# Performance work log

Measured on AMD Instinct MI355X. Metric: run time of the kernel, lower is better.

Reference implementation:

```python
import jax, jax.numpy as jnp
import numpy as np

B, S, D_MODEL, N_HEADS, HIDDEN = 4, 2048, 1024, 16, 4096
D_HEAD = D_MODEL // N_HEADS
LN_EPS = 1e-5


def setup_inputs() -> dict:
    key = jax.random.key(0)
    ks = jax.random.split(key, 20)
    s = 0.02
    return {
        "X": jax.random.normal(ks[0], (B, S, D_MODEL), dtype=jnp.float32),
        # attention projections (stored [in, out]; y = x @ W + b)
        "Wq": jax.random.normal(ks[1], (D_MODEL, D_MODEL), dtype=jnp.float32) * s,
        "bq": jnp.zeros((D_MODEL,), jnp.float32),
        "Wk": jax.random.normal(ks[2], (D_MODEL, D_MODEL), dtype=jnp.float32) * s,
        "bk": jnp.zeros((D_MODEL,), jnp.float32),
        "Wv": jax.random.normal(ks[3], (D_MODEL, D_MODEL), dtype=jnp.float32) * s,
        "bv": jnp.zeros((D_MODEL,), jnp.float32),
        "Wo": jax.random.normal(ks[4], (D_MODEL, D_MODEL), dtype=jnp.float32) * s,
        "bo": jnp.zeros((D_MODEL,), jnp.float32),
        # layernorm 1
        "g1": jnp.ones((D_MODEL,), jnp.float32),
        "beta1": jnp.zeros((D_MODEL,), jnp.float32),
        # FFN
        "W1": jax.random.normal(ks[5], (D_MODEL, HIDDEN), dtype=jnp.float32) * s,
        "b1": jnp.zeros((HIDDEN,), jnp.float32),
        "W2": jax.random.normal(ks[6], (HIDDEN, D_MODEL), dtype=jnp.float32) * s,
        "b2": jnp.zeros((D_MODEL,), jnp.float32),
        # layernorm 2
        "g2": jnp.ones((D_MODEL,), jnp.float32),
        "beta2": jnp.zeros((D_MODEL,), jnp.float32),
    }


def _layer_norm(x, gamma, beta):
    mu = jnp.mean(x, axis=-1, keepdims=True)
    var = jnp.mean(jnp.square(x - mu), axis=-1, keepdims=True)
    return (x - mu) * jax.lax.rsqrt(var + LN_EPS) * gamma + beta


def reference(X, Wq, bq, Wk, bk, Wv, bv, Wo, bo, g1, beta1, W1, b1, W2, b2, g2, beta2):
    b, s, d = X.shape
    # multi-head attention (dropout is identity in eval mode)
    q = (X @ Wq + bq).reshape(b, s, N_HEADS, D_HEAD)
    k = (X @ Wk + bk).reshape(b, s, N_HEADS, D_HEAD)
    v = (X @ Wv + bv).reshape(b, s, N_HEADS, D_HEAD)
    scale = 1.0 / np.sqrt(D_HEAD).astype(np.float32)
    scores = jnp.einsum('bqhd,bkhd->bhqk', q, k) * scale
    attn = jax.nn.softmax(scores, axis=-1)
    ctx = jnp.einsum('bhqk,bkhd->bqhd', attn, v).reshape(b, s, d)
    attn_out = ctx @ Wo + bo
    # AddNorm 1
    Y = _layer_norm(X + attn_out, g1, beta1)
    # FFN
    ffn_out = jax.nn.relu(Y @ W1 + b1) @ W2 + b2
    # AddNorm 2
    return _layer_norm(Y + ffn_out, g2, beta2)
```

## Files before the change

### kernel.cpp

```cpp
#include <hip/hip_runtime.h>
#include <stdint.h>

typedef unsigned short u16;
typedef short bf16x8 __attribute__((ext_vector_type(8)));
typedef float f32x4 __attribute__((ext_vector_type(4)));
typedef u16 u16x4 __attribute__((ext_vector_type(4)));
typedef u16 u16x8 __attribute__((ext_vector_type(8)));

#define LOG2E 1.4426950408889634f
#define QSCALE (0.125f * LOG2E)

__device__ __forceinline__ u16 f2bf(float f) {
  union { float f; uint32_t u; } x; x.f = f;
  uint32_t r = x.u + 0x7fffu + ((x.u >> 16) & 1u);
  return (u16)(r >> 16);
}
__device__ __forceinline__ u16 f2bf_ru(float f) {
  union { float f; uint32_t u; } x; x.f = f;
  return (u16)((x.u + 0x8000u) >> 16);
}
__device__ __forceinline__ float bf2f(u16 h) {
  union { uint32_t u; float f; } x; x.u = ((uint32_t)h) << 16;
  return x.f;
}
__device__ __forceinline__ uint32_t cvtpk(float lo, float hi) {
  uint32_t r;
  asm("v_cvt_pk_bf16_f32 %0, %1, %2" : "=v"(r) : "v"(lo), "v"(hi));
  return r;
}
__device__ __forceinline__ int swz3(int row) { return (row ^ (row >> 3)) & 7; }

__device__ __forceinline__ void gload_lds16(const void* g, void* lds) {
  __builtin_amdgcn_global_load_lds(
      (const __attribute__((address_space(1))) void*)g,
      (__attribute__((address_space(3))) void*)lds, 16, 0, 0);
}

__global__ __launch_bounds__(256) void cast_bf16(const float* __restrict__ in,
                                                 u16* __restrict__ out, int n8) {
  int i = blockIdx.x * 256 + threadIdx.x;
  const int stride = gridDim.x * 256;
  for (; i < n8; i += stride) {
    const f32x4* p = (const f32x4*)in + (size_t)i * 2;
    f32x4 a = p[0], b = p[1];
    u16x8 o;
    o[0] = f2bf(a[0]); o[1] = f2bf(a[1]); o[2] = f2bf(a[2]); o[3] = f2bf(a[3]);
    o[4] = f2bf(b[0]); o[5] = f2bf(b[1]); o[6] = f2bf(b[2]); o[7] = f2bf(b[3]);
    ((u16x8*)out)[i] = o;
  }
}

__global__ __launch_bounds__(256) void concat3(const float* __restrict__ a,
                                               const float* __restrict__ b,
                                               const float* __restrict__ c,
                                               float* __restrict__ o) {
  int i = blockIdx.x * 256 + threadIdx.x;
  if (i < 3072)
    o[i] = i < 1024 ? a[i] * QSCALE : (i < 2048 ? b[i - 1024] : c[i - 2048]);
}

__global__ __launch_bounds__(256) void transpose_cast(const float* __restrict__ in,
                                                      u16* __restrict__ out, int R, int C,
                                                      float scale) {
  __shared__ float tile[32][33];
  const int bc = blockIdx.x * 32, br = blockIdx.y * 32;
  const int tx = threadIdx.x & 31, ty = threadIdx.x >> 5;
#pragma unroll
  for (int i = 0; i < 32; i += 8)
    tile[ty + i][tx] = in[(size_t)(br + ty + i) * C + bc + tx];
  __syncthreads();
#pragma unroll
  for (int i = 0; i < 32; i += 8)
    out[(size_t)(bc + ty + i) * R + br + tx] = f2bf(tile[tx][ty + i] * scale);
}

__global__ __launch_bounds__(256) void vtrans(const u16* __restrict__ QKV,
                                              u16* __restrict__ Vtg) {
  __shared__ u16 tl[64][65];
  const int t = threadIdx.x;
  const int sblk = blockIdx.x, h = blockIdx.y, b = blockIdx.z;
  const int s0 = sblk * 64;
  const size_t ibase = ((size_t)b * 2048) * 3072 + 2048 + h * 64;
#pragma unroll
  for (int i = 0; i < 2; i++) {
    const int idx = i * 256 + t;
    const int sl = idx >> 3, d0 = (idx & 7) * 8;
    bf16x8 v = *(const bf16x8*)&QKV[ibase + (size_t)(s0 + sl) * 3072 + d0];
#pragma unroll
    for (int e = 0; e < 8; e++) tl[d0 + e][sl] = (u16)v[e];
  }
  __syncthreads();
  const size_t ob = ((size_t)(b * 16 + h) * 64) * 2048;
#pragma unroll
  for (int i = 0; i < 2; i++) {
    const int idx = i * 256 + t;
    const int r = idx >> 3, c0 = (idx & 7) * 8;
    u16x8 o;
#pragma unroll
    for (int e = 0; e < 8; e++) o[e] = tl[r][c0 + e];
    *(u16x8*)&Vtg[ob + (size_t)r * 2048 + s0 + c0] = o;
  }
}

template <int RELU>
__global__ __launch_bounds__(256) void gemm_bt(const u16* __restrict__ A,
                                               const u16* __restrict__ BT,
                                               const float* __restrict__ bias,
                                               u16* __restrict__ Cb,
                                               int M, int N, int K) {
  constexpr int BM = 128, BN = 128, BK = 64;
  __shared__ u16 As[BM * BK];
  __shared__ u16 Bs[BN * BK];
  const int t = threadIdx.x;
  const int w = t >> 6, lane = t & 63;
  const int la = lane & 15, lb = lane >> 4;
  const int wr = w >> 1, wc = w & 1;
  const int m0 = blockIdx.y * BM, n0 = blockIdx.x * BN;

  f32x4 acc[4][4];
#pragma unroll
  for (int i = 0; i < 4; i++)
#pragma unroll
    for (int j = 0; j < 4; j++) acc[i][j] = (f32x4){0.f, 0.f, 0.f, 0.f};

  for (int kt = 0; kt < K; kt += BK) {
#pragma unroll
    for (int i = 0; i < 4; i++) {
      const int s = i * 256 + t;
      const int row = s >> 3, col = (s & 7) * 8;
      gload_lds16(A + (size_t)(m0 + row) * K + kt + col, &As[(i * 256 + w * 64) * 8]);
      gload_lds16(BT + (size_t)(n0 + row) * K + kt + col, &Bs[(i * 256 + w * 64) * 8]);
    }
    __syncthreads();
#pragma unroll
    for (int ks = 0; ks < 2; ks++) {
      bf16x8 af[4], bfr[4];
#pragma unroll
      for (int i = 0; i < 4; i++)
        af[i] = *(const bf16x8*)&As[(wr * 64 + i * 16 + la) * BK + ks * 32 + lb * 8];
#pragma unroll
      for (int j = 0; j < 4; j++)
        bfr[j] = *(const bf16x8*)&Bs[(wc * 64 + j * 16 + la) * BK + ks * 32 + lb * 8];
#pragma unroll
      for (int i = 0; i < 4; i++)
#pragma unroll
        for (int j = 0; j < 4; j++)
          acc[i][j] = __builtin_amdgcn_mfma_f32_16x16x32_bf16(af[i], bfr[j], acc[i][j], 0, 0, 0);
    }
    __syncthreads();
  }
#pragma unroll
  for (int i = 0; i < 4; i++) {
    const int r = m0 + wr * 64 + i * 16 + lb * 4;
#pragma unroll
    for (int j = 0; j < 4; j++) {
      const int c = n0 + wc * 64 + j * 16 + la;
      const float bv = bias[c];
#pragma unroll
      for (int rr = 0; rr < 4; rr++) {
        float v = acc[i][j][rr] + bv;
        if (RELU) v = fmaxf(v, 0.f);
        Cb[(size_t)(r + rr) * N + c] = f2bf(v);
      }
    }
  }
}

template <int RELU>
__global__ __launch_bounds__(512, 2) void gemm8p(const u16* __restrict__ A,
                                                 const u16* __restrict__ BT,
                                                 const float* __restrict__ bias,
                                                 u16* __restrict__ Cb,
                                                 int M, int N, int K, int nbx) {
  __shared__ u16 As[2][256 * 64];
  __shared__ u16 Bs[2][256 * 64];
  const int t = threadIdx.x;
  const int w = t >> 6, lane = t & 63;
  const int la = lane & 15, lb = lane >> 4;
  const int wr = w >> 2, wc = w & 3;
  int bid = (int)blockIdx.x;
  const int cpx = (int)gridDim.x >> 3;
  bid = (bid & 7) * cpx + (bid >> 3);
  const int m0 = (bid / nbx) * 256, n0 = (bid % nbx) * 256;
  const int NT = K >> 6;
  const int row64 = t >> 3;
  const int colp = ((t & 7) ^ swz3(row64)) << 3;

#define STG_A(buf, tile, q) \
  gload_lds16(A + (size_t)(m0 + (q)*64 + row64) * K + ((tile) << 6) + colp, \
              &As[buf][(q)*4096 + w * 512])
#define STG_B(buf, tile, q) \
  gload_lds16(BT + (size_t)(n0 + (q)*64 + row64) * K + ((tile) << 6) + colp, \
              &Bs[buf][(q)*4096 + w * 512])
#define LDA(dst, mf, ks) { const int r_ = wr * 128 + (mf)*16 + la; \
  dst = *(const bf16x8*)&As[cur][r_ * 64 + (((((ks) << 2) + lb) ^ swz3(r_)) << 3)]; }
#define LDB(dst, nf, ks) { const int r_ = wc * 64 + (nf)*16 + la; \
  dst = *(const bf16x8*)&Bs[cur][r_ * 64 + (((((ks) << 2) + lb) ^ swz3(r_)) << 3)]; }
#define MFMA16(mh, nh, barr) \
  __builtin_amdgcn_s_setprio(1); \
  _Pragma("unroll") for (int ks = 0; ks < 2; ks++) \
  _Pragma("unroll") for (int i = 0; i < 4; i++) \
  _Pragma("unroll") for (int j = 0; j < 2; j++) \
    acc[(mh)*4 + i][(nh)*2 + j] = __builtin_amdgcn_mfma_f32_16x16x32_bf16( \
        af[i][ks], barr[j][ks], acc[(mh)*4 + i][(nh)*2 + j], 0, 0, 0); \
  __builtin_amdgcn_s_setprio(0);
#define BAR1() __builtin_amdgcn_s_barrier(); \
  asm volatile("s_waitcnt lgkmcnt(0)" ::: "memory"); \
  __builtin_amdgcn_sched_barrier(0)

  f32x4 acc[8][4];
#pragma unroll
  for (int i = 0; i < 8; i++)
#pragma unroll
    for (int j = 0; j < 4; j++) acc[i][j] = (f32x4){0.f, 0.f, 0.f, 0.f};

  STG_A(0, 0, 0); STG_A(0, 0, 2);
  STG_B(0, 0, 0); STG_B(0, 0, 1); STG_B(0, 0, 2); STG_B(0, 0, 3);
  STG_A(0, 0, 1); STG_A(0, 0, 3);
  asm volatile("s_waitcnt vmcnt(2)" ::: "memory");
  __builtin_amdgcn_s_barrier();

  for (int tile = 0; tile < NT; ++tile) {
    const int cur = tile & 1, nxt = cur ^ 1;
    const bool hn = (tile + 1) < NT;
    bf16x8 af[4][2], b0[2][2], b1[2][2];
#pragma unroll
    for (int i = 0; i < 4; i++) { LDA(af[i][0], i, 0); LDA(af[i][1], i, 1); }
#pragma unroll
    for (int j = 0; j < 2; j++) { LDB(b0[j][0], j, 0); LDB(b0[j][1], j, 1); }
    if (hn) { STG_A(nxt, tile + 1, 0); STG_A(nxt, tile + 1, 2); }
    BAR1();
    MFMA16(0, 0, b0);
    __builtin_amdgcn_s_barrier();
#pragma unroll
    for (int j = 0; j < 2; j++) { LDB(b1[j][0], 2 + j, 0); LDB(b1[j][1], 2 + j, 1); }
    if (hn) { STG_B(nxt, tile + 1, 0); STG_B(nxt, tile + 1, 1); }
    BAR1();
    MFMA16(0, 1, b1);
    if (hn) { asm volatile("s_waitcnt vmcnt(4)" ::: "memory"); }
    else    { asm volatile("s_waitcnt vmcnt(0)" ::: "memory"); }
    __builtin_amdgcn_s_barrier();
#pragma unroll
    for (int i = 0; i < 4; i++) { LDA(af[i][0], 4 + i, 0); LDA(af[i][1], 4 + i, 1); }
    if (hn) { STG_B(nxt, tile + 1, 2); STG_B(nxt, tile + 1, 3); }
    BAR1();
    MFMA16(1, 0, b0);
    __builtin_amdgcn_s_barrier();
    if (hn) { STG_A(nxt, tile + 1, 1); STG_A(nxt, tile + 1, 3); }
    BAR1();
    MFMA16(1, 1, b1);
    if (hn) { asm volatile("s_waitcnt vmcnt(2)" ::: "memory"); }
    __builtin_amdgcn_s_barrier();
  }
#undef STG_A
#undef STG_B
#undef LDA
#undef LDB
#undef MFMA16
#undef BAR1

#pragma unroll
  for (int mf = 0; mf < 8; mf++) {
    const int r = m0 + wr * 128 + mf * 16 + lb * 4;
#pragma unroll
    for (int nf = 0; nf < 4; nf++) {
      const int c = n0 + wc * 64 + nf * 16 + la;
      const float bv = bias[c];
#pragma unroll
      for (int rr = 0; rr < 4; rr++) {
        float v = acc[mf][nf][rr] + bv;
        if (RELU) v = fmaxf(v, 0.f);
        Cb[(size_t)(r + rr) * N + c] = f2bf(v);
      }
    }
  }
}

__global__ __launch_bounds__(256) void attn_fwd(const u16* __restrict__ Qg,
                                                const u16* __restrict__ Kg,
                                                const u16* __restrict__ Vtg,
                                                u16* __restrict__ Og, int LDM) {
  constexpr int S = 2048, DMO = 1024, NT = S / 64;
  __shared__ u16 Ks[2][64 * 64];
  __shared__ u16 Vt[2][64 * 64];
  const int t = threadIdx.x, w = t >> 6, lane = t & 63;
  const int la = lane & 15, lb = lane >> 4;
  const int qb = blockIdx.x, h = blockIdx.y, b = blockIdx.z;
  const size_t base = ((size_t)b * S) * LDM + h * 64;
  const size_t vbase = ((size_t)(b * 16 + h) * 64) * 2048;
  const size_t obase = ((size_t)b * S) * DMO + h * 64;
  const int qrow0 = qb * 128 + w * 32;
  const int sl0 = la + 32 * (lb & 1), sl1 = sl0 + 16;
  const int jsel = lb >> 1;

#define ATT_STAGE(buf, kt_) { \
  _Pragma("unroll") for (int i = 0; i < 2; i++) { \
    const int s = i * 256 + t; const int r = s >> 3; const int cg = s & 7; \
    gload_lds16(Kg + base + (size_t)((kt_) + r) * LDM + ((cg ^ swz3(r)) << 3), \
                &Ks[buf][s * 8]); } \
  _Pragma("unroll") for (int i = 0; i < 2; i++) { \
    const int s = i * 256 + t; const int r = s >> 3; const int cg = s & 7; \
    gload_lds16(Vtg + vbase + (size_t)r * 2048 + (kt_) + ((cg ^ swz3(r)) << 3), \
                &Vt[buf][s * 8]); } }

  bf16x8 qf[2][2];
#pragma unroll
  for (int rf = 0; rf < 2; rf++)
#pragma unroll
    for (int ks = 0; ks < 2; ks++)
      qf[rf][ks] = *(const bf16x8*)&Qg[base + (size_t)(qrow0 + rf * 16 + la) * LDM + ks * 32 + lb * 8];

  f32x4 accO[2][4];
  float m[2], l[2];
#pragma unroll
  for (int i = 0; i < 2; i++) {
    m[i] = -1e30f; l[i] = 0.f;
#pragma unroll
    for (int j = 0; j < 4; j++) accO[i][j] = (f32x4){0.f, 0.f, 0.f, 0.f};
  }

  ATT_STAGE(0, 0);
  asm volatile("s_waitcnt vmcnt(0)" ::: "memory");
  __builtin_amdgcn_s_barrier();

  for (int kt = 0; kt < NT; ++kt) {
    const int cur = kt & 1;
    if (kt + 1 < NT) ATT_STAGE(cur ^ 1, (kt + 1) * 64);

    f32x4 st[4][2];
#pragma unroll
    for (int j = 0; j < 4; j++)
#pragma unroll
      for (int rf = 0; rf < 2; rf++) st[j][rf] = (f32x4){0.f, 0.f, 0.f, 0.f};
    __builtin_amdgcn_s_setprio(1);
#pragma unroll
    for (int ks = 0; ks < 2; ks++) {
      bf16x8 kf[4];
#pragma unroll
      for (int j = 0; j < 4; j++) {
        const int r = j * 16 + la;
        kf[j] = *(const bf16x8*)&Ks[cur][r * 64 + ((((ks << 2) + lb) ^ swz3(r)) << 3)];
      }
#pragma unroll
      for (int j = 0; j < 4; j++)
#pragma unroll
        for (int rf = 0; rf < 2; rf++)
          st[j][rf] = __builtin_amdgcn_mfma_f32_16x16x32_bf16(kf[j], qf[rf][ks], st[j][rf], 0, 0, 0);
    }
    __builtin_amdgcn_s_setprio(0);

    bf16x8 pf[2][2];
#pragma unroll
    for (int rf = 0; rf < 2; rf++) {
      float rm = st[0][rf][0];
#pragma unroll
      for (int j = 0; j < 4; j++)
#pragma unroll
        for (int rr = 0; rr < 4; rr++) rm = fmaxf(rm, st[j][rf][rr]);
      if (__any(rm > m[rf] + 8.0f)) {
        rm = fmaxf(rm, __shfl_xor(rm, 16, 64));
        rm = fmaxf(rm, __shfl_xor(rm, 32, 64));
        const float mN = fmaxf(m[rf], rm);
        const float al = exp2f(m[rf] - mN);
        m[rf] = mN;
        l[rf] *= al;
#pragma unroll
        for (int rr = 0; rr < 4; rr++) {
          const float alr = __shfl(al, (lb << 2) + rr, 64);
#pragma unroll
          for (int cf = 0; cf < 4; cf++) accO[rf][cf][rr] *= alr;
        }
      }
      uint32_t wl[4], wh[4];
#pragma unroll
      for (int j = 0; j < 4; j++) {
        float p0 = exp2f(st[j][rf][0] - m[rf]);
        float p1 = exp2f(st[j][rf][1] - m[rf]);
        float p2 = exp2f(st[j][rf][2] - m[rf]);
        float p3 = exp2f(st[j][rf][3] - m[rf]);
        l[rf] += (p0 + p1) + (p2 + p3);
        wl[j] = cvtpk(p0, p1);
        wh[j] = cvtpk(p2, p3);
      }
#pragma unroll
      for (int ks = 0; ks < 2; ks++) {
        const int j0 = 2 * ks, j1 = 2 * ks + 1;
        uint32_t a0 = __shfl(wl[j0], sl0, 64), a1 = __shfl(wh[j0], sl0, 64);
        uint32_t a2 = __shfl(wl[j0], sl1, 64), a3 = __shfl(wh[j0], sl1, 64);
        uint32_t b0 = __shfl(wl[j1], sl0, 64), b1 = __shfl(wh[j1], sl0, 64);
        uint32_t b2 = __shfl(wl[j1], sl1, 64), b3 = __shfl(wh[j1], sl1, 64);
        union { uint32_t u[4]; bf16x8 v; } pk;
        pk.u[0] = jsel ? b0 : a0;
        pk.u[1] = jsel ? b1 : a1;
        pk.u[2] = jsel ? b2 : a2;
        pk.u[3] = jsel ? b3 : a3;
        pf[rf][ks] = pk.v;
      }
    }

    __builtin_amdgcn_s_setprio(1);
#pragma unroll
    for (int ks = 0; ks < 2; ks++) {
      bf16x8 vf[4];
#pragma unroll
      for (int cf = 0; cf < 4; cf++) {
        const int dr = cf * 16 + la;
        vf[cf] = *(const bf16x8*)&Vt[cur][dr * 64 + ((((ks << 2) + lb) ^ swz3(dr)) << 3)];
      }
#pragma unroll
      for (int rf = 0; rf < 2; rf++)
#pragma unroll
        for (int cf = 0; cf < 4; cf++)
          accO[rf][cf] = __builtin_amdgcn_mfma_f32_16x16x32_bf16(pf[rf][ks], vf[cf], accO[rf][cf], 0, 0, 0);
    }
    __builtin_amdgcn_s_setprio(0);

    asm volatile("s_waitcnt vmcnt(0)" ::: "memory");
    __builtin_amdgcn_s_barrier();
  }
#undef ATT_STAGE

#pragma unroll
  for (int rf = 0; rf < 2; rf++) {
    float l2 = l[rf];
    l2 += __shfl_xor(l2, 16, 64);
    l2 += __shfl_xor(l2, 32, 64);
    const float inv = 1.0f / l2;
#pragma unroll
    for (int rr = 0; rr < 4; rr++) {
      const float invr = __shfl(inv, (lb << 2) + rr, 64);
      const int r = qrow0 + rf * 16 + lb * 4 + rr;
#pragma unroll
      for (int cf = 0; cf < 4; cf++)
        Og[obase + (size_t)r * DMO + cf * 16 + la] = f2bf_ru(accO[rf][cf][rr] * invr);
    }
  }
}

template <int AF32, int OUTF32>
__global__ __launch_bounds__(256) void add_ln(const void* __restrict__ Ap,
                                              const u16* __restrict__ Bb,
                                              const float* __restrict__ g,
                                              const float* __restrict__ be,
                                              void* __restrict__ Yp) {
  constexpr int D = 1024;
  const int row = blockIdx.x, t = threadIdx.x;
  f32x4 a;
  if (AF32) {
    a = ((const f32x4*)((const float*)Ap + (size_t)row * D))[t];
  } else {
    u16x4 av = ((const u16x4*)((const u16*)Ap + (size_t)row * D))[t];
#pragma unroll
    for (int i = 0; i < 4; i++) a[i] = bf2f(av[i]);
  }
  u16x4 bv16 = ((const u16x4*)(Bb + (size_t)row * D))[t];
  f32x4 x;
#pragma unroll
  for (int i = 0; i < 4; i++) x[i] = a[i] + bf2f(bv16[i]);
  float s1 = x[0] + x[1] + x[2] + x[3];
  float s2 = x[0] * x[0] + x[1] * x[1] + x[2] * x[2] + x[3] * x[3];
#pragma unroll
  for (int off = 32; off > 0; off >>= 1) {
    s1 += __shfl_down(s1, off, 64);
    s2 += __shfl_down(s2, off, 64);
  }
  __shared__ float sm[8];
  const int w = t >> 6, lane = t & 63;
  if (lane == 0) { sm[w] = s1; sm[4 + w] = s2; }
  __syncthreads();
  s1 = sm[0] + sm[1] + sm[2] + sm[3];
  s2 = sm[4] + sm[5] + sm[6] + sm[7];
  const float mean = s1 * (1.0f / D);
  const float var = s2 * (1.0f / D) - mean * mean;
  const float rstd = rsqrtf(var + 1e-5f);
  const f32x4 gv = ((const f32x4*)g)[t];
  const f32x4 bv = ((const f32x4*)be)[t];
  f32x4 y;
#pragma unroll
  for (int i = 0; i < 4; i++) y[i] = (x[i] - mean) * rstd * gv[i] + bv[i];
  if (OUTF32) {
    ((f32x4*)((float*)Yp + (size_t)row * D))[t] = y;
  } else {
    u16x4 o;
#pragma unroll
    for (int i = 0; i < 4; i++) o[i] = f2bf(y[i]);
    ((u16x4*)((u16*)Yp + (size_t)row * D))[t] = o;
  }
}

extern "C" void kernel_launch(void* const* d_in, const int* in_sizes, int n_in,
                              void* d_out, int out_size, void* d_ws, size_t ws_size,
                              hipStream_t stream) {
  const float* X   = (const float*)d_in[0];
  const float* Wq  = (const float*)d_in[1];
  const float* bq  = (const float*)d_in[2];
  const float* Wk  = (const float*)d_in[3];
  const float* bk  = (const float*)d_in[4];
  const float* Wv  = (const float*)d_in[5];
  const float* bv  = (const float*)d_in[6];
  const float* Wo  = (const float*)d_in[7];
  const float* bo  = (const float*)d_in[8];
  const float* g1  = (const float*)d_in[9];
  const float* be1 = (const float*)d_in[10];
  const float* W1  = (const float*)d_in[11];
  const float* b1  = (const float*)d_in[12];
  const float* W2  = (const float*)d_in[13];
  const float* b2  = (const float*)d_in[14];
  const float* g2  = (const float*)d_in[15];
  const float* be2 = (const float*)d_in[16];

  const size_t MB = 1ull << 20;
  char* wsb = (char*)d_ws;
  u16*   WqkvT = (u16*)(wsb + 0 * MB);
  u16*   WoT   = (u16*)(wsb + 6 * MB);
  u16*   W1T   = (u16*)(wsb + 8 * MB);
  u16*   W2T   = (u16*)(wsb + 16 * MB);
  u16*   Xb    = (u16*)(wsb + 24 * MB);
  u16*   Ab    = (u16*)(wsb + 24 * MB);
  u16*   Fb    = (u16*)(wsb + 24 * MB);
  u16*   QKVb  = (u16*)(wsb + 40 * MB);
  u16*   Hb    = (u16*)(wsb + 40 * MB);
  float* bqkv  = (float*)(wsb + 88 * MB);
  u16*   Cx    = (u16*)(wsb + 88 * MB);
  u16*   Vt_g  = (u16*)(wsb + 104 * MB);
  u16*   Yb    = (u16*)(wsb + 104 * MB);
  (void)ws_size; (void)in_sizes; (void)n_in; (void)out_size;

  cast_bf16<<<2048, 256, 0, stream>>>(X, Xb, 8192 * 1024 / 8);
  concat3<<<12, 256, 0, stream>>>(bq, bk, bv, bqkv);
  transpose_cast<<<dim3(32, 32), 256, 0, stream>>>(Wq, WqkvT, 1024, 1024, QSCALE);
  transpose_cast<<<dim3(32, 32), 256, 0, stream>>>(Wk, WqkvT + 1024 * 1024, 1024, 1024, 1.0f);
  transpose_cast<<<dim3(32, 32), 256, 0, stream>>>(Wv, WqkvT + 2 * 1024 * 1024, 1024, 1024, 1.0f);
  transpose_cast<<<dim3(32, 32), 256, 0, stream>>>(Wo, WoT, 1024, 1024, 1.0f);
  transpose_cast<<<dim3(128, 32), 256, 0, stream>>>(W1, W1T, 1024, 4096, 1.0f);
  transpose_cast<<<dim3(32, 128), 256, 0, stream>>>(W2, W2T, 4096, 1024, 1.0f);

  gemm8p<0><<<384, 512, 0, stream>>>(Xb, WqkvT, bqkv, QKVb, 8192, 3072, 1024, 12);

  vtrans<<<dim3(32, 16, 4), 256, 0, stream>>>(QKVb, Vt_g);
  attn_fwd<<<dim3(16, 16, 4), 256, 0, stream>>>(QKVb, QKVb + 1024, Vt_g, Cx, 3072);

  gemm_bt<0><<<dim3(8, 64), 256, 0, stream>>>(Cx, WoT, bo, Ab, 8192, 1024, 1024);
  add_ln<1, 0><<<8192, 256, 0, stream>>>(X, Ab, g1, be1, Yb);
  gemm8p<1><<<512, 512, 0, stream>>>(Yb, W1T, b1, Hb, 8192, 4096, 1024, 16);
  gemm_bt<0><<<dim3(8, 64), 256, 0, stream>>>(Hb, W2T, b2, Fb, 8192, 1024, 4096);
  add_ln<0, 1><<<8192, 256, 0, stream>>>(Yb, Fb, g2, be2, d_out);
}
```

Baseline: 489.3 us.

## Switch attention to 32x32x16 MFMA with permlane P repack and MFMA row sums

Rewrites the attention inner loop to use 32x32x16 bf16 MFMAs, so each wave handles one 32-row query tile with a single running max instead of two 16-row tiles. The P matrix is repacked for the PV product with v_permlane32_swap instead of many cross-lane shuffles. The softmax denominator is accumulated by an extra MFMA against a ones vector instead of scalar adds. A launch-bounds occupancy hint of 3 is added. This aims to cut shuffle and VALU overhead in the softmax stage, at the cost of an extra MFMA per k-block and bf16-rounded row sums.

```diff
diff --git a/kernel.cpp b/kernel.cpp
--- a/kernel.cpp
+++ b/kernel.cpp
@@ -4,6 +4,7 @@
 typedef unsigned short u16;
 typedef short bf16x8 __attribute__((ext_vector_type(8)));
 typedef float f32x4 __attribute__((ext_vector_type(4)));
+typedef float f32x16 __attribute__((ext_vector_type(16)));
 typedef u16 u16x4 __attribute__((ext_vector_type(4)));
 typedef u16 u16x8 __attribute__((ext_vector_type(8)));
 
@@ -276,22 +277,20 @@
   }
 }
 
-__global__ __launch_bounds__(256) void attn_fwd(const u16* __restrict__ Qg,
-                                                const u16* __restrict__ Kg,
-                                                const u16* __restrict__ Vtg,
-                                                u16* __restrict__ Og, int LDM) {
+__global__ __launch_bounds__(256, 3) void attn_fwd(const u16* __restrict__ Qg,
+                                                   const u16* __restrict__ Kg,
+                                                   const u16* __restrict__ Vtg,
+                                                   u16* __restrict__ Og, int LDM) {
   constexpr int S = 2048, DMO = 1024, NT = S / 64;
   __shared__ u16 Ks[2][64 * 64];
   __shared__ u16 Vt[2][64 * 64];
   const int t = threadIdx.x, w = t >> 6, lane = t & 63;
-  const int la = lane & 15, lb = lane >> 4;
+  const int l5 = lane & 31, hf = lane >> 5;
   const int qb = blockIdx.x, h = blockIdx.y, b = blockIdx.z;
   const size_t base = ((size_t)b * S) * LDM + h * 64;
   const size_t vbase = ((size_t)(b * 16 + h) * 64) * 2048;
   const size_t obase = ((size_t)b * S) * DMO + h * 64;
   const int qrow0 = qb * 128 + w * 32;
-  const int sl0 = la + 32 * (lb & 1), sl1 = sl0 + 16;
-  const int jsel = lb >> 1;
 
 #define ATT_STAGE(buf, kt_) { \
   _Pragma("unroll") for (int i = 0; i < 2; i++) { \
@@ -303,21 +302,19 @@
     gload_lds16(Vtg + vbase + (size_t)r * 2048 + (kt_) + ((cg ^ swz3(r)) << 3), \
                 &Vt[buf][s * 8]); } }
 
-  bf16x8 qf[2][2];
-#pragma unroll
-  for (int rf = 0; rf < 2; rf++)
-#pragma unroll
-    for (int ks = 0; ks < 2; ks++)
-      qf[rf][ks] = *(const bf16x8*)&Qg[base + (size_t)(qrow0 + rf * 16 + la) * LDM + ks * 32 + lb * 8];
-
-  f32x4 accO[2][4];
-  float m[2], l[2];
-#pragma unroll
-  for (int i = 0; i < 2; i++) {
-    m[i] = -1e30f; l[i] = 0.f;
-#pragma unroll
-    for (int j = 0; j < 4; j++) accO[i][j] = (f32x4){0.f, 0.f, 0.f, 0.f};
-  }
+  bf16x8 qf[4];
+#pragma unroll
+  for (int kb = 0; kb < 4; kb++)
+    qf[kb] = *(const bf16x8*)&Qg[base + (size_t)(qrow0 + l5) * LDM + kb * 16 + hf * 8];
+
+  f32x16 accO0, accO1, accL;
+#pragma unroll
+  for (int i = 0; i < 16; i++) { accO0[i] = 0.f; accO1[i] = 0.f; accL[i] = 0.f; }
+  float m = -1e30f;
+
+  bf16x8 ones;
+#pragma unroll
+  for (int i = 0; i < 8; i++) ones[i] = (short)0x3F80;
 
   ATT_STAGE(0, 0);
   asm volatile("s_waitcnt vmcnt(0)" ::: "memory");
@@ -327,91 +324,75 @@
     const int cur = kt & 1;
     if (kt + 1 < NT) ATT_STAGE(cur ^ 1, (kt + 1) * 64);
 
-    f32x4 st[4][2];
-#pragma unroll
-    for (int j = 0; j < 4; j++)
-#pragma unroll
-      for (int rf = 0; rf < 2; rf++) st[j][rf] = (f32x4){0.f, 0.f, 0.f, 0.f};
+    f32x16 st0, st1;
+#pragma unroll
+    for (int i = 0; i < 16; i++) { st0[i] = 0.f; st1[i] = 0.f; }
     __builtin_amdgcn_s_setprio(1);
 #pragma unroll
-    for (int ks = 0; ks < 2; ks++) {
-      bf16x8 kf[4];
-#pragma unroll
-      for (int j = 0; j < 4; j++) {
-        const int r = j * 16 + la;
-        kf[j] = *(const bf16x8*)&Ks[cur][r * 64 + ((((ks << 2) + lb) ^ swz3(r)) << 3)];
+    for (int kb = 0; kb < 4; kb++) {
+      const int r0 = l5, r1 = 32 + l5;
+      bf16x8 kf0 = *(const bf16x8*)&Ks[cur][r0 * 64 + (((hf + 2 * kb) ^ swz3(r0)) << 3)];
+      bf16x8 kf1 = *(const bf16x8*)&Ks[cur][r1 * 64 + (((hf + 2 * kb) ^ swz3(r1)) << 3)];
+      st0 = __builtin_amdgcn_mfma_f32_32x32x16_bf16(kf0, qf[kb], st0, 0, 0, 0);
+      st1 = __builtin_amdgcn_mfma_f32_32x32x16_bf16(kf1, qf[kb], st1, 0, 0, 0);
+    }
+    __builtin_amdgcn_s_setprio(0);
+
+    float rm = st0[0];
+#pragma unroll
+    for (int i = 1; i < 16; i++) rm = fmaxf(rm, st0[i]);
+#pragma unroll
+    for (int i = 0; i < 16; i++) rm = fmaxf(rm, st1[i]);
+    if (__any(rm > m + 8.0f)) {
+      float ra = rm, rb = rm;
+      asm volatile("v_permlane32_swap_b32 %0, %1" : "+v"(ra), "+v"(rb));
+      rm = fmaxf(rm, fmaxf(ra, rb));
+      const float mN = fmaxf(m, rm);
+      const float al = exp2f(m - mN);
+      m = mN;
+#pragma unroll
+      for (int r = 0; r < 16; r++) {
+        const float alr = __shfl(al, (r & 3) + 8 * (r >> 2) + 4 * hf, 64);
+        accO0[r] *= alr; accO1[r] *= alr; accL[r] *= alr;
       }
-#pragma unroll
-      for (int j = 0; j < 4; j++)
-#pragma unroll
-        for (int rf = 0; rf < 2; rf++)
-          st[j][rf] = __builtin_amdgcn_mfma_f32_16x16x32_bf16(kf[j], qf[rf][ks], st[j][rf], 0, 0, 0);
-    }
-    __builtin_amdgcn_s_setprio(0);
-
-    bf16x8 pf[2][2];
-#pragma unroll
-    for (int rf = 0; rf < 2; rf++) {
-      float rm = st[0][rf][0];
-#pragma unroll
-      for (int j = 0; j < 4; j++)
-#pragma unroll
-        for (int rr = 0; rr < 4; rr++) rm = fmaxf(rm, st[j][rf][rr]);
-      if (__any(rm > m[rf] + 8.0f)) {
-        rm = fmaxf(rm, __shfl_xor(rm, 16, 64));
-        rm = fmaxf(rm, __shfl_xor(rm, 32, 64));
-        const float mN = fmaxf(m[rf], rm);
-        const float al = exp2f(m[rf] - mN);
-        m[rf] = mN;
-        l[rf] *= al;
-#pragma unroll
-        for (int rr = 0; rr < 4; rr++) {
-          const float alr = __shfl(al, (lb << 2) + rr, 64);
-#pragma unroll
-          for (int cf = 0; cf < 4; cf++) accO[rf][cf][rr] *= alr;
-        }
-      }
-      uint32_t wl[4], wh[4];
-#pragma unroll
-      for (int j = 0; j < 4; j++) {
-        float p0 = exp2f(st[j][rf][0] - m[rf]);
-        float p1 = exp2f(st[j][rf][1] - m[rf]);
-        float p2 = exp2f(st[j][rf][2] - m[rf]);
-        float p3 = exp2f(st[j][rf][3] - m[rf]);
-        l[rf] += (p0 + p1) + (p2 + p3);
-        wl[j] = cvtpk(p0, p1);
-        wh[j] = cvtpk(p2, p3);
-      }
-#pragma unroll
-      for (int ks = 0; ks < 2; ks++) {
-        const int j0 = 2 * ks, j1 = 2 * ks + 1;
-        uint32_t a0 = __shfl(wl[j0], sl0, 64), a1 = __shfl(wh[j0], sl0, 64);
-        uint32_t a2 = __shfl(wl[j0], sl1, 64), a3 = __shfl(wh[j0], sl1, 64);
-        uint32_t b0 = __shfl(wl[j1], sl0, 64), b1 = __shfl(wh[j1], sl0, 64);
-        uint32_t b2 = __shfl(wl[j1], sl1, 64), b3 = __shfl(wh[j1], sl1, 64);
-        union { uint32_t u[4]; bf16x8 v; } pk;
-        pk.u[0] = jsel ? b0 : a0;
-        pk.u[1] = jsel ? b1 : a1;
-        pk.u[2] = jsel ? b2 : a2;
-        pk.u[3] = jsel ? b3 : a3;
-        pf[rf][ks] = pk.v;
-      }
+    }
+
+    uint32_t pw0[8], pw1[8];
+#pragma unroll
+    for (int r2 = 0; r2 < 8; r2++) {
+      pw0[r2] = cvtpk(exp2f(st0[2 * r2] - m), exp2f(st0[2 * r2 + 1] - m));
+      pw1[r2] = cvtpk(exp2f(st1[2 * r2] - m), exp2f(st1[2 * r2 + 1] - m));
+    }
+    bf16x8 pf[4];
+    {
+      uint32_t a0 = pw0[0], b0v = pw0[2], a1 = pw0[1], b1v = pw0[3];
+      asm volatile("v_permlane32_swap_b32 %0, %1" : "+v"(a0), "+v"(b0v));
+      asm volatile("v_permlane32_swap_b32 %0, %1" : "+v"(a1), "+v"(b1v));
+      union { uint32_t u[4]; bf16x8 v; } k;
+      k.u[0] = a0; k.u[1] = a1; k.u[2] = b0v; k.u[3] = b1v; pf[0] = k.v;
+      uint32_t c0 = pw0[4], d0 = pw0[6], c1 = pw0[5], d1 = pw0[7];
+      asm volatile("v_permlane32_swap_b32 %0, %1" : "+v"(c0), "+v"(d0));
+      asm volatile("v_permlane32_swap_b32 %0, %1" : "+v"(c1), "+v"(d1));
+      k.u[0] = c0; k.u[1] = c1; k.u[2] = d0; k.u[3] = d1; pf[1] = k.v;
+      uint32_t e0 = pw1[0], f0 = pw1[2], e1 = pw1[1], f1 = pw1[3];
+      asm volatile("v_permlane32_swap_b32 %0, %1" : "+v"(e0), "+v"(f0));
+      asm volatile("v_permlane32_swap_b32 %0, %1" : "+v"(e1), "+v"(f1));
+      k.u[0] = e0; k.u[1] = e1; k.u[2] = f0; k.u[3] = f1; pf[2] = k.v;
+      uint32_t g0 = pw1[4], h0 = pw1[6], g1 = pw1[5], h1 = pw1[7];
+      asm volatile("v_permlane32_swap_b32 %0, %1" : "+v"(g0), "+v"(h0));
+      asm volatile("v_permlane32_swap_b32 %0, %1" : "+v"(g1), "+v"(h1));
+      k.u[0] = g0; k.u[1] = g1; k.u[2] = h0; k.u[3] = h1; pf[3] = k.v;
     }
 
     __builtin_amdgcn_s_setprio(1);
 #pragma unroll
-    for (int ks = 0; ks < 2; ks++) {
-      bf16x8 vf[4];
-#pragma unroll
-      for (int cf = 0; cf < 4; cf++) {
-        const int dr = cf * 16 + la;
-        vf[cf] = *(const bf16x8*)&Vt[cur][dr * 64 + ((((ks << 2) + lb) ^ swz3(dr)) << 3)];
-      }
-#pragma unroll
-      for (int rf = 0; rf < 2; rf++)
-#pragma unroll
-        for (int cf = 0; cf < 4; cf++)
-          accO[rf][cf] = __builtin_amdgcn_mfma_f32_16x16x32_bf16(pf[rf][ks], vf[cf], accO[rf][cf], 0, 0, 0);
+    for (int kb = 0; kb < 4; kb++) {
+      const int r0 = l5, r1 = 32 + l5;
+      bf16x8 vf0 = *(const bf16x8*)&Vt[cur][r0 * 64 + (((hf + 2 * kb) ^ swz3(r0)) << 3)];
+      bf16x8 vf1 = *(const bf16x8*)&Vt[cur][r1 * 64 + (((hf + 2 * kb) ^ swz3(r1)) << 3)];
+      accO0 = __builtin_amdgcn_mfma_f32_32x32x16_bf16(pf[kb], vf0, accO0, 0, 0, 0);
+      accO1 = __builtin_amdgcn_mfma_f32_32x32x16_bf16(pf[kb], vf1, accO1, 0, 0, 0);
+      accL  = __builtin_amdgcn_mfma_f32_32x32x16_bf16(pf[kb], ones, accL, 0, 0, 0);
     }
     __builtin_amdgcn_s_setprio(0);
 
@@ -421,19 +402,11 @@
 #undef ATT_STAGE
 
 #pragma unroll
-  for (int rf = 0; rf < 2; rf++) {
-    float l2 = l[rf];
-    l2 += __shfl_xor(l2, 16, 64);
-    l2 += __shfl_xor(l2, 32, 64);
-    const float inv = 1.0f / l2;
-#pragma unroll
-    for (int rr = 0; rr < 4; rr++) {
-      const float invr = __shfl(inv, (lb << 2) + rr, 64);
-      const int r = qrow0 + rf * 16 + lb * 4 + rr;
-#pragma unroll
-      for (int cf = 0; cf < 4; cf++)
-        Og[obase + (size_t)r * DMO + cf * 16 + la] = f2bf_ru(accO[rf][cf][rr] * invr);
-    }
+  for (int r = 0; r < 16; r++) {
+    const float inv = 1.0f / accL[r];
+    const int row = qrow0 + (r & 3) + 8 * (r >> 2) + 4 * hf;
+    Og[obase + (size_t)row * DMO + l5]      = f2bf_ru(accO0[r] * inv);
+    Og[obase + (size_t)row * DMO + 32 + l5] = f2bf_ru(accO1[r] * inv);
   }
 }
 
```

After: 447.2 us. 8.6% less time.
